# Performance work log

Hardware: AMD Instinct MI355X
Metric: run time of the kernel (lower is better)

The kernel has to match this reference:

```python
import jax, jax.numpy as jnp
import numpy as np

NUM_HEADS = 16
NEG_INF = -1e30


def setup_inputs() -> dict:
    key = jax.random.key(0)
    k1, k2, k3 = jax.random.split(key, 3)
    B, S, D = 2, 2048, 1024
    x = jax.random.normal(k1, (B, S, D), dtype=jnp.float32)
    # torch Linear(D, 3D, bias=False) stored here already transposed: y = x @ w_qkv
    w_qkv = jax.random.normal(k2, (D, 3 * D), dtype=jnp.float32) * 0.02
    w_out = jax.random.normal(k3, (D, D), dtype=jnp.float32) * 0.02
    return {"x": x, "w_qkv": w_qkv, "w_out": w_out}


def reference(x, w_qkv, w_out):
    B, S, D = x.shape
    H = NUM_HEADS
    dh = D // H
    qkv = x @ w_qkv                      # [B, S, 3D]
    q, k, v = jnp.split(qkv, 3, axis=-1)

    def to_heads(t):
        return t.reshape(B, S, H, dh).transpose(0, 2, 1, 3)  # [B, H, S, dh]

    q, k, v = to_heads(q), to_heads(k), to_heads(v)
    scale = jnp.asarray(dh, x.dtype) ** -0.5
    scores = jnp.einsum('bhqd,bhkd->bhqk', q, k) * scale     # [B, H, S, S]
    causal = jnp.tril(jnp.ones((S, S), dtype=bool))
    scores = jnp.where(causal, scores, NEG_INF)
    attn = jax.nn.softmax(scores, axis=-1)
    out = jnp.einsum('bhqk,bhkd->bhqd', attn, v)             # [B, H, S, dh]
    out = out.transpose(0, 2, 1, 3).reshape(B, S, D)
    return out @ w_out
```

## Files before the change

### kernel.cpp

```cpp
#include <hip/hip_runtime.h>

typedef unsigned short u16;
typedef unsigned int u32;

typedef __bf16 bf16x8 __attribute__((ext_vector_type(8)));
typedef _Float16 f16x8 __attribute__((ext_vector_type(8)));
typedef float f32x4 __attribute__((ext_vector_type(4)));
typedef float f32x16 __attribute__((ext_vector_type(16)));
typedef u32 u32x4 __attribute__((ext_vector_type(4)));

typedef __attribute__((address_space(1))) u32 as1_u32;
typedef __attribute__((address_space(3))) u32 as3_u32;

#define EKF 0.18033688011112042f

__device__ __forceinline__ u16 f2bf(float x) {
  u32 u = __float_as_uint(x);
  u = u + 0x7fffu + ((u >> 16) & 1u);
  return (u16)(u >> 16);
}
__device__ __forceinline__ u32 pack2(float a, float b) {
  return (u32)f2bf(a) | ((u32)f2bf(b) << 16);
}
__device__ __forceinline__ u32 pkf16(float a, float b) {
  return __builtin_bit_cast(u32, __builtin_amdgcn_cvt_pkrtz(a, b));
}
__device__ __forceinline__ u16 f2h(float a) {
  return (u16)(pkf16(a, a) & 0xffffu);
}
__device__ __forceinline__ void gld_lds16(const u16* g, const u16* l) {
  __builtin_amdgcn_global_load_lds((const as1_u32*)g, (as3_u32*)l, 16, 0, 0);
}

__global__ __launch_bounds__(256) void prepass_kernel(const float* __restrict__ x,
                                                      const float* __restrict__ w_qkv,
                                                      const float* __restrict__ w_out,
                                                      u16* __restrict__ xb,
                                                      u16* __restrict__ wqkvT,
                                                      u16* __restrict__ woutT) {
  __shared__ float tile[64][65];
  int bid = blockIdx.x;
  int t = threadIdx.x;
  if (bid < 4096) {
    int i = bid * 256 + t;
    float4 v = ((const float4*)x)[i];
    uint2 r;
    r.x = pack2(v.x, v.y);
    r.y = pack2(v.z, v.w);
    ((uint2*)xb)[i] = r;
    return;
  }
  const float* W;
  u16* WT;
  int K, N, bx, by;
  if (bid < 4096 + 768) {
    int b2 = bid - 4096;
    W = w_qkv; WT = wqkvT; K = 1024; N = 3072; bx = b2 & 15; by = b2 >> 4;
  } else {
    int b2 = bid - 4864;
    W = w_out; WT = woutT; K = 1024; N = 1024; bx = b2 & 15; by = b2 >> 4;
  }
  int k0 = bx * 64, n0 = by * 64;
  int r = t >> 4, c4 = (t & 15) * 4;
#pragma unroll
  for (int i = 0; i < 4; ++i) {
    int row = r + i * 16;
    float4 v = *(const float4*)&W[(size_t)(k0 + row) * N + n0 + c4];
    tile[row][c4 + 0] = v.x; tile[row][c4 + 1] = v.y;
    tile[row][c4 + 2] = v.z; tile[row][c4 + 3] = v.w;
  }
  __syncthreads();
#pragma unroll
  for (int i = 0; i < 4; ++i) {
    int n = r + i * 16;
    uint2 o;
    o.x = pack2(tile[c4 + 0][n], tile[c4 + 1][n]);
    o.y = pack2(tile[c4 + 2][n], tile[c4 + 3][n]);
    *(uint2*)&WT[(size_t)(n0 + n) * K + k0 + c4] = o;
  }
}

__global__ __launch_bounds__(512, 2) void gemm_qkv256_kernel(const u16* __restrict__ A,
                                                             const u16* __restrict__ BT,
                                                             u16* __restrict__ QK,
                                                             u16* __restrict__ VT) {
  __shared__ __attribute__((aligned(16))) u16 smem[57344];
  const int tid = threadIdx.x;
  const int wave = tid >> 6;
  const int lane = tid & 63;
  const int lr = lane & 15;
  const int kg = lane >> 4;
  const int l7 = lr & 7;
  const int wr = wave >> 2;
  const int wc = wave & 3;

  int b = blockIdx.x;
  int sw = (b & 7) * 32 + (b >> 3);
  const int bm = (sw >> 4) * 256;
  const int bn = (sw & 15) * 192;

  const int srow = tid >> 3;
  const int scg = ((tid & 7) ^ (srow & 7)) * 8;
  const u16* pa = A + (size_t)(bm + srow) * 1024 + scg;
  const u16* pb = BT + (size_t)(bn + srow) * 1024 + scg;
  const u32 lw = (u32)wave * 512;

  f32x4 acc[8][3];
#pragma unroll
  for (int i = 0; i < 8; ++i)
#pragma unroll
    for (int j = 0; j < 3; ++j) {
      f32x4 z = {0.f, 0.f, 0.f, 0.f};
      acc[i][j] = z;
    }

  {
    u16* dA = (u16*)smem;
    u16* dB = (u16*)smem + 16384;
#pragma unroll
    for (int i = 0; i < 4; ++i) gld_lds16(pa + (size_t)(i * 64) * 1024, dA + lw + i * 4096);
#pragma unroll
    for (int i = 0; i < 3; ++i) gld_lds16(pb + (size_t)(i * 64) * 1024, dB + lw + i * 4096);
  }

  for (int t = 0; t < 16; ++t) {
    __syncthreads();
    const u16* bA = smem + (t & 1) * 28672;
    const u16* bB = bA + 16384;
    if (t + 1 < 16) {
      u16* dA = (u16*)smem + ((t + 1) & 1) * 28672;
      u16* dB = dA + 16384;
      const int k1 = (t + 1) * 64;
#pragma unroll
      for (int i = 0; i < 4; ++i) gld_lds16(pa + (size_t)(i * 64) * 1024 + k1, dA + lw + i * 4096);
#pragma unroll
      for (int i = 0; i < 3; ++i) gld_lds16(pb + (size_t)(i * 64) * 1024 + k1, dB + lw + i * 4096);
    }
    bf16x8 bfr[2][3];
#pragma unroll
    for (int kh = 0; kh < 2; ++kh)
#pragma unroll
      for (int ni = 0; ni < 3; ++ni)
        bfr[kh][ni] = *(const bf16x8*)(bB + (wc * 48 + ni * 16 + lr) * 64 +
                                       (((kh * 4 + kg) ^ l7) * 8));
#pragma unroll
    for (int ph = 0; ph < 4; ++ph) {
      const int mh = ph >> 1, kh = ph & 1;
      bf16x8 af[4];
#pragma unroll
      for (int mi = 0; mi < 4; ++mi)
        af[mi] = *(const bf16x8*)(bA + (wr * 128 + mh * 64 + mi * 16 + lr) * 64 +
                                  (((kh * 4 + kg) ^ l7) * 8));
      __builtin_amdgcn_s_barrier();
      __builtin_amdgcn_s_setprio(1);
#pragma unroll
      for (int mi = 0; mi < 4; ++mi)
#pragma unroll
        for (int ni = 0; ni < 3; ++ni)
          acc[mh * 4 + mi][ni] = __builtin_amdgcn_mfma_f32_16x16x32_bf16(
              bfr[kh][ni], af[mi], acc[mh * 4 + mi][ni], 0, 0, 0);
      __builtin_amdgcn_s_setprio(0);
      __builtin_amdgcn_s_barrier();
    }
  }

  __syncthreads();
#pragma unroll
  for (int i = 0; i < 8; ++i)
#pragma unroll
    for (int ni = 0; ni < 3; ++ni) {
      const int coff = wc * 48 + ni * 16 + kg * 4;
      const int cglob = bn + coff;
      f32x4 a = acc[i][ni];
      if (cglob >= 2048) {
        int r = bm + wr * 128 + i * 16 + lr;
        int cc = cglob - 2048;
        int bh2 = (r >> 11) * 16 + (cc >> 6);
        int j = r & 2047;
        u16* vrow = VT + ((size_t)bh2 * 64 + (cc & 63)) * 2048 + j;
#pragma unroll
        for (int rr = 0; rr < 4; ++rr) vrow[(size_t)rr * 2048] = f2h(a[rr]);
      } else {
        float scale = (cglob < 1024) ? EKF : 1.0f;
        int row = wr * 128 + i * 16 + lr;
        int chunk = coff >> 2;
        u32 off = (u32)row * 192 + (u32)((chunk ^ (row & 6)) << 2);
        *(uint2*)((u16*)smem + off) =
            make_uint2(pack2(a[0] * scale, a[1] * scale), pack2(a[2] * scale, a[3] * scale));
      }
    }
  __syncthreads();
  if (bn < 2048) {
#pragma unroll
    for (int i2 = 0; i2 < 16; ++i2) {
      int row = i2 * 16 + (tid >> 5);
      int lc = tid & 31;
      if (lc < 24 && bn + lc * 8 < 2048) {
        uint4 v = *(const uint4*)((const u16*)smem + (u32)row * 192 +
                                  (u32)(((2 * lc) ^ (row & 6)) * 4));
        *(uint4*)(QK + (size_t)(bm + row) * 2048 + bn + lc * 8) = v;
      }
    }
  }
}

__global__ __launch_bounds__(256, 2) void gemm_out_kernel(const u16* __restrict__ A,
                                                          const u16* __restrict__ BT,
                                                          float* __restrict__ C) {
  __shared__ __attribute__((aligned(16))) u16 smem[2][12288];
  const int tid = threadIdx.x;
  const int wave = tid >> 6;
  const int lane = tid & 63;
  const int lr = lane & 15;
  const int kg = lane >> 4;
  const int lr7 = lr & 7;
  const int wm = (wave >> 1) * 32;
  const int wn = (wave & 1) * 64;

  const int b = blockIdx.x;
  const int xcd = b & 7, loc = b >> 3;
  const int bm = (xcd * 8 + (loc >> 3)) * 64;
  const int bn = (loc & 7) * 128;

  const int sr = tid >> 3;
  const int scg = ((tid & 7) ^ (sr & 7)) * 8;
  const u16* pa = A + (size_t)(bm + sr) * 1024 + scg;
  const u16* pb = BT + (size_t)(bn + sr) * 1024 + scg;
  const u32 lw = (u32)wave * 512;

  f32x4 acc[2][4];
#pragma unroll
  for (int i = 0; i < 2; ++i)
#pragma unroll
    for (int j = 0; j < 4; ++j) {
      f32x4 z = {0.f, 0.f, 0.f, 0.f};
      acc[i][j] = z;
    }

  {
    u16* dA = smem[0];
    u16* dB = smem[0] + 4096;
#pragma unroll
    for (int i = 0; i < 2; ++i) gld_lds16(pa + (size_t)(i * 32) * 1024, dA + lw + i * 2048);
#pragma unroll
    for (int i = 0; i < 4; ++i) gld_lds16(pb + (size_t)(i * 32) * 1024, dB + lw + i * 2048);
  }

  for (int t = 0; t < 16; ++t) {
    __syncthreads();
    const u16* bA = smem[t & 1];
    const u16* bB = bA + 4096;
    if (t + 1 < 16) {
      u16* dA = smem[(t + 1) & 1];
      u16* dB = dA + 4096;
      const int k1 = (t + 1) * 64;
#pragma unroll
      for (int i = 0; i < 2; ++i) gld_lds16(pa + (size_t)(i * 32) * 1024 + k1, dA + lw + i * 2048);
#pragma unroll
      for (int i = 0; i < 4; ++i) gld_lds16(pb + (size_t)(i * 32) * 1024 + k1, dB + lw + i * 2048);
    }
#pragma unroll
    for (int kk = 0; kk < 2; ++kk) {
      const int ch = ((kk * 4 + kg) ^ lr7) * 8;
      bf16x8 af[2], bfr[4];
#pragma unroll
      for (int mi = 0; mi < 2; ++mi)
        af[mi] = *(const bf16x8*)(bA + (wm + mi * 16 + lr) * 64 + ch);
#pragma unroll
      for (int ni = 0; ni < 4; ++ni)
        bfr[ni] = *(const bf16x8*)(bB + (wn + ni * 16 + lr) * 64 + ch);
      __builtin_amdgcn_s_setprio(1);
#pragma unroll
      for (int mi = 0; mi < 2; ++mi)
#pragma unroll
        for (int ni = 0; ni < 4; ++ni)
          acc[mi][ni] = __builtin_amdgcn_mfma_f32_16x16x32_bf16(bfr[ni], af[mi], acc[mi][ni], 0, 0, 0);
      __builtin_amdgcn_s_setprio(0);
    }
  }

  float* buf = (float*)smem;
#pragma unroll
  for (int hc = 0; hc < 2; ++hc) {
    __syncthreads();
    if ((wave & 1) == hc) {
#pragma unroll
      for (int mi = 0; mi < 2; ++mi)
#pragma unroll
        for (int ni = 0; ni < 4; ++ni) {
          int row = wm + mi * 16 + lr;
          int cp = ((ni * 4 + kg) ^ lr) * 4;
          *(f32x4*)(buf + row * 64 + cp) = acc[mi][ni];
        }
    }
    __syncthreads();
#pragma unroll
    for (int i = 0; i < 4; ++i) {
      int row = i * 16 + (tid >> 4);
      int lc = tid & 15;
      float4 v = *(const float4*)(buf + row * 64 + ((lc ^ (row & 15)) * 4));
      *(float4*)(C + (size_t)(bm + row) * 1024 + bn + hc * 64 + lc * 4) = v;
    }
  }
}

__global__ __launch_bounds__(256, 4) void attn_mfma_kernel(const u16* __restrict__ qk,
                                                           const u16* __restrict__ vt,
                                                           u16* __restrict__ out) {
  __shared__ __attribute__((aligned(16))) u16 sK[2][64 * 64];
  __shared__ __attribute__((aligned(16))) u16 sV[2][64 * 64];

  const int tid = threadIdx.x;
  const int wave = tid >> 6;
  const int lane = tid & 63;
  const int l31 = lane & 31;
  const int hi = lane >> 5;
  const int qh = wave & 1;
  const int jh = wave >> 1;

  int idx = blockIdx.x;
  int qi = 31 - (idx >> 5);
  int bh = (idx & 7) * 4 + ((idx >> 3) & 3);
  int b = bh >> 4, h = bh & 15;
  int q0 = qi * 64;

  const u16* qbase = qk + (size_t)b * 2048 * 2048 + h * 64;
  const u16* kbase = qbase + 1024;
  const u16* vbase = vt + (size_t)bh * 64 * 2048;
  u16* obase = out + (size_t)b * 2048 * 1024 + h * 64;

  const int sra = wave * 16 + (lane >> 3);
  const int srb = sra + 8;
  const int sc = lane & 7;
  const u32 koffA = (u32)sra * 2048 + (u32)((sc ^ (sra & 7)) * 8);
  const u32 koffB = (u32)srb * 2048 + (u32)((sc ^ (srb & 7)) * 8);
  const u32 ldsA = (wave * 2 + 0) * 512;
  const u32 ldsB = (wave * 2 + 1) * 512;

  const int qcol = q0 + qh * 32 + l31;
  bf16x8 qf[4];
  {
    const u16* qrow = qbase + (size_t)qcol * 2048;
#pragma unroll
    for (int s = 0; s < 4; ++s) qf[s] = *(const bf16x8*)(qrow + s * 16 + hi * 8);
  }

  f32x16 oacc[2];
#pragma unroll
  for (int i = 0; i < 16; ++i) { oacc[0][i] = 0.f; oacc[1][i] = 0.f; }
  float ls = 0.f;

  const int nrounds = qi + 1;
  gld_lds16(kbase + koffA, sK[0] + ldsA);
  gld_lds16(kbase + koffB, sK[0] + ldsB);
  gld_lds16(vbase + koffA, sV[0] + ldsA);
  gld_lds16(vbase + koffB, sV[0] + ldsB);
  __syncthreads();

  for (int t = 0; t < nrounds; ++t) {
    if (t + 1 < nrounds) {
      int j1 = (t + 1) * 64;
      u16* dK = sK[(t + 1) & 1];
      u16* dV = sV[(t + 1) & 1];
      gld_lds16(kbase + (size_t)j1 * 2048 + koffA, dK + ldsA);
      gld_lds16(kbase + (size_t)j1 * 2048 + koffB, dK + ldsB);
      gld_lds16(vbase + j1 + koffA, dV + ldsA);
      gld_lds16(vbase + j1 + koffB, dV + ldsB);
    }
    const u16* sKb = sK[t & 1];
    const u16* sVb = sV[t & 1];
    const bool diag = (t == qi);

    f32x16 c;
#pragma unroll
    for (int i = 0; i < 16; ++i) c[i] = 0.f;
#pragma unroll
    for (int s = 0; s < 4; ++s) {
      const u32 row = (u32)(jh * 32 + l31);
      bf16x8 kf = *(const bf16x8*)(sKb + row * 64 + (((2 * s + hi) ^ (row & 7)) * 8));
      c = __builtin_amdgcn_mfma_f32_32x32x16_bf16(kf, qf[s], c, 0, 0, 0);
    }
    float p[16];
    const int qrel = qh * 32 + l31;
#pragma unroll
    for (int r = 0; r < 16; ++r) {
      int joff = jh * 32 + (r & 3) + 8 * (r >> 2) + 4 * hi;
      float e = exp2f(c[r]);
      p[r] = (!diag || (joff <= qrel)) ? e : 0.f;
    }
    {
      float s0 = (p[0] + p[1]) + (p[2] + p[3]);
      float s1 = (p[4] + p[5]) + (p[6] + p[7]);
      float s2 = (p[8] + p[9]) + (p[10] + p[11]);
      float s3 = (p[12] + p[13]) + (p[14] + p[15]);
      ls += (s0 + s1) + (s2 + s3);
    }
    u32 c01 = pkf16(p[0], p[1]),   c23 = pkf16(p[2], p[3]);
    u32 c45 = pkf16(p[4], p[5]),   c67 = pkf16(p[6], p[7]);
    u32 c89 = pkf16(p[8], p[9]),   cab = pkf16(p[10], p[11]);
    u32 ccd = pkf16(p[12], p[13]), cef = pkf16(p[14], p[15]);
    asm volatile("v_permlane32_swap_b32 %0, %1" : "+v"(c01), "+v"(c45));
    asm volatile("v_permlane32_swap_b32 %0, %1" : "+v"(c23), "+v"(c67));
    asm volatile("v_permlane32_swap_b32 %0, %1" : "+v"(c89), "+v"(ccd));
    asm volatile("v_permlane32_swap_b32 %0, %1" : "+v"(cab), "+v"(cef));
    u32x4 w0 = {c01, c23, c45, c67};
    u32x4 w1 = {c89, cab, ccd, cef};
    f16x8 pa0 = __builtin_bit_cast(f16x8, w0);
    f16x8 pa1 = __builtin_bit_cast(f16x8, w1);

    __builtin_amdgcn_s_setprio(1);
#pragma unroll
    for (int dh = 0; dh < 2; ++dh) {
      const u32 row = (u32)(dh * 32 + l31);
#pragma unroll
      for (int s2 = 0; s2 < 2; ++s2) {
        f16x8 vf = *(const f16x8*)(sVb + row * 64 +
                                   (((4 * jh + 2 * s2 + hi) ^ (row & 7)) * 8));
        oacc[dh] = __builtin_amdgcn_mfma_f32_32x32x16_f16(
            vf, (s2 == 0) ? pa0 : pa1, oacc[dh], 0, 0, 0);
      }
    }
    __builtin_amdgcn_s_setprio(0);
    __syncthreads();
  }

  ls += __shfl_xor(ls, 32);

  float* obuf = (float*)sK;
  float* lbuf = (float*)sV;
  const int q = qh * 32 + l31;
  if (jh == 1) {
#pragma unroll
    for (int dh = 0; dh < 2; ++dh)
#pragma unroll
      for (int g = 0; g < 4; ++g) {
        int ch = dh * 8 + g * 2 + hi;
        f32x4 w = {oacc[dh][4 * g + 0], oacc[dh][4 * g + 1],
                   oacc[dh][4 * g + 2], oacc[dh][4 * g + 3]};
        *(f32x4*)(obuf + q * 64 + ((ch ^ (q & 15)) * 4)) = w;
      }
    if (hi == 0) lbuf[q] = ls;
  }
  __syncthreads();
  if (jh == 0) {
    float inv = 1.0f / (ls + lbuf[q]);
    u16* orow = obase + (size_t)qcol * 1024;
#pragma unroll
    for (int dh = 0; dh < 2; ++dh)
#pragma unroll
      for (int g = 0; g < 4; ++g) {
        int ch = dh * 8 + g * 2 + hi;
        f32x4 po = *(const f32x4*)(obuf + q * 64 + ((ch ^ (q & 15)) * 4));
        float o0 = (oacc[dh][4 * g + 0] + po[0]) * inv;
        float o1 = (oacc[dh][4 * g + 1] + po[1]) * inv;
        float o2 = (oacc[dh][4 * g + 2] + po[2]) * inv;
        float o3 = (oacc[dh][4 * g + 3] + po[3]) * inv;
        *(uint2*)(orow + dh * 32 + g * 8 + hi * 4) = make_uint2(pack2(o0, o1), pack2(o2, o3));
      }
  }
}

extern "C" void kernel_launch(void* const* d_in, const int* in_sizes, int n_in,
                              void* d_out, int out_size, void* d_ws, size_t ws_size,
                              hipStream_t stream) {
  const float* x = (const float*)d_in[0];
  const float* w_qkv = (const float*)d_in[1];
  const float* w_out = (const float*)d_in[2];
  float* out = (float*)d_out;

  char* ws = (char*)d_ws;
  u16* xb    = (u16*)(ws);
  u16* wqkvT = (u16*)(ws + (8u << 20));
  u16* woutT = (u16*)(ws + (14u << 20));
  u16* qkb   = (u16*)(ws + (16u << 20));
  u16* vtb   = (u16*)(ws + (32u << 20));
  u16* attn  = (u16*)(ws + (40u << 20));

  prepass_kernel<<<5120, 256, 0, stream>>>(x, w_qkv, w_out, xb, wqkvT, woutT);

  gemm_qkv256_kernel<<<256, 512, 0, stream>>>(xb, wqkvT, qkb, vtb);

  attn_mfma_kernel<<<1024, 256, 0, stream>>>(qkb, vtb, attn);

  gemm_out_kernel<<<512, 256, 0, stream>>>(attn, woutT, out);
}
```

Before: 160.5 us.

## Shrink QKV GEMM tile to 128 rows and drop intra-tile barriers

The QKV projection GEMM tile drops from 256x192 to 128x192, so 512 blocks are launched instead of 256 and shared memory per block is smaller, allowing higher occupancy (launch bounds raised to 4). The inner loop is simplified to two k-halves without the per-phase s_barrier synchronisation, and the block-to-tile mapping is changed to group rows per XCD. This aims to fill the 256 CUs better and cut barrier stalls, at the cost of less B-tile reuse per loaded A and more global traffic for the weight tile.

```diff
diff --git a/kernel.cpp b/kernel.cpp
--- a/kernel.cpp
+++ b/kernel.cpp
@@ -80,11 +80,11 @@
   }
 }
 
-__global__ __launch_bounds__(512, 2) void gemm_qkv256_kernel(const u16* __restrict__ A,
+__global__ __launch_bounds__(512, 4) void gemm_qkv128_kernel(const u16* __restrict__ A,
                                                              const u16* __restrict__ BT,
                                                              u16* __restrict__ QK,
                                                              u16* __restrict__ VT) {
-  __shared__ __attribute__((aligned(16))) u16 smem[57344];
+  __shared__ __attribute__((aligned(16))) u16 smem[40960];
   const int tid = threadIdx.x;
   const int wave = tid >> 6;
   const int lane = tid & 63;
@@ -94,10 +94,10 @@
   const int wr = wave >> 2;
   const int wc = wave & 3;
 
-  int b = blockIdx.x;
-  int sw = (b & 7) * 32 + (b >> 3);
-  const int bm = (sw >> 4) * 256;
-  const int bn = (sw & 15) * 192;
+  const int b = blockIdx.x;
+  const int xcd = b & 7, loc = b >> 3;
+  const int bm = (xcd * 4 + (loc >> 4)) * 128;
+  const int bn = (loc & 15) * 192;
 
   const int srow = tid >> 3;
   const int scg = ((tid & 7) ^ (srow & 7)) * 8;
@@ -105,9 +105,9 @@
   const u16* pb = BT + (size_t)(bn + srow) * 1024 + scg;
   const u32 lw = (u32)wave * 512;
 
-  f32x4 acc[8][3];
-#pragma unroll
-  for (int i = 0; i < 8; ++i)
+  f32x4 acc[4][3];
+#pragma unroll
+  for (int i = 0; i < 4; ++i)
 #pragma unroll
     for (int j = 0; j < 3; ++j) {
       f32x4 z = {0.f, 0.f, 0.f, 0.f};
@@ -116,64 +116,56 @@
 
   {
     u16* dA = (u16*)smem;
-    u16* dB = (u16*)smem + 16384;
-#pragma unroll
-    for (int i = 0; i < 4; ++i) gld_lds16(pa + (size_t)(i * 64) * 1024, dA + lw + i * 4096);
+    u16* dB = (u16*)smem + 8192;
+#pragma unroll
+    for (int i = 0; i < 2; ++i) gld_lds16(pa + (size_t)(i * 64) * 1024, dA + lw + i * 4096);
 #pragma unroll
     for (int i = 0; i < 3; ++i) gld_lds16(pb + (size_t)(i * 64) * 1024, dB + lw + i * 4096);
   }
 
   for (int t = 0; t < 16; ++t) {
     __syncthreads();
-    const u16* bA = smem + (t & 1) * 28672;
-    const u16* bB = bA + 16384;
+    const u16* bA = smem + (t & 1) * 20480;
+    const u16* bB = bA + 8192;
     if (t + 1 < 16) {
-      u16* dA = (u16*)smem + ((t + 1) & 1) * 28672;
-      u16* dB = dA + 16384;
+      u16* dA = (u16*)smem + ((t + 1) & 1) * 20480;
+      u16* dB = dA + 8192;
       const int k1 = (t + 1) * 64;
 #pragma unroll
-      for (int i = 0; i < 4; ++i) gld_lds16(pa + (size_t)(i * 64) * 1024 + k1, dA + lw + i * 4096);
+      for (int i = 0; i < 2; ++i) gld_lds16(pa + (size_t)(i * 64) * 1024 + k1, dA + lw + i * 4096);
 #pragma unroll
       for (int i = 0; i < 3; ++i) gld_lds16(pb + (size_t)(i * 64) * 1024 + k1, dB + lw + i * 4096);
     }
-    bf16x8 bfr[2][3];
-#pragma unroll
-    for (int kh = 0; kh < 2; ++kh)
+#pragma unroll
+    for (int kk = 0; kk < 2; ++kk) {
+      const int ch = ((kk * 4 + kg) ^ l7) * 8;
+      bf16x8 af[4], bfr[3];
+#pragma unroll
+      for (int mi = 0; mi < 4; ++mi)
+        af[mi] = *(const bf16x8*)(bA + (wr * 64 + mi * 16 + lr) * 64 + ch);
 #pragma unroll
       for (int ni = 0; ni < 3; ++ni)
-        bfr[kh][ni] = *(const bf16x8*)(bB + (wc * 48 + ni * 16 + lr) * 64 +
-                                       (((kh * 4 + kg) ^ l7) * 8));
-#pragma unroll
-    for (int ph = 0; ph < 4; ++ph) {
-      const int mh = ph >> 1, kh = ph & 1;
-      bf16x8 af[4];
+        bfr[ni] = *(const bf16x8*)(bB + (wc * 48 + ni * 16 + lr) * 64 + ch);
+      __builtin_amdgcn_s_setprio(1);
 #pragma unroll
       for (int mi = 0; mi < 4; ++mi)
-        af[mi] = *(const bf16x8*)(bA + (wr * 128 + mh * 64 + mi * 16 + lr) * 64 +
-                                  (((kh * 4 + kg) ^ l7) * 8));
-      __builtin_amdgcn_s_barrier();
-      __builtin_amdgcn_s_setprio(1);
-#pragma unroll
-      for (int mi = 0; mi < 4; ++mi)
 #pragma unroll
         for (int ni = 0; ni < 3; ++ni)
-          acc[mh * 4 + mi][ni] = __builtin_amdgcn_mfma_f32_16x16x32_bf16(
-              bfr[kh][ni], af[mi], acc[mh * 4 + mi][ni], 0, 0, 0);
+          acc[mi][ni] = __builtin_amdgcn_mfma_f32_16x16x32_bf16(bfr[ni], af[mi], acc[mi][ni], 0, 0, 0);
       __builtin_amdgcn_s_setprio(0);
-      __builtin_amdgcn_s_barrier();
     }
   }
 
   __syncthreads();
 #pragma unroll
-  for (int i = 0; i < 8; ++i)
+  for (int i = 0; i < 4; ++i)
 #pragma unroll
     for (int ni = 0; ni < 3; ++ni) {
       const int coff = wc * 48 + ni * 16 + kg * 4;
       const int cglob = bn + coff;
       f32x4 a = acc[i][ni];
       if (cglob >= 2048) {
-        int r = bm + wr * 128 + i * 16 + lr;
+        int r = bm + wr * 64 + i * 16 + lr;
         int cc = cglob - 2048;
         int bh2 = (r >> 11) * 16 + (cc >> 6);
         int j = r & 2047;
@@ -182,7 +174,7 @@
         for (int rr = 0; rr < 4; ++rr) vrow[(size_t)rr * 2048] = f2h(a[rr]);
       } else {
         float scale = (cglob < 1024) ? EKF : 1.0f;
-        int row = wr * 128 + i * 16 + lr;
+        int row = wr * 64 + i * 16 + lr;
         int chunk = coff >> 2;
         u32 off = (u32)row * 192 + (u32)((chunk ^ (row & 6)) << 2);
         *(uint2*)((u16*)smem + off) =
@@ -192,7 +184,7 @@
   __syncthreads();
   if (bn < 2048) {
 #pragma unroll
-    for (int i2 = 0; i2 < 16; ++i2) {
+    for (int i2 = 0; i2 < 8; ++i2) {
       int row = i2 * 16 + (tid >> 5);
       int lc = tid & 31;
       if (lc < 24 && bn + lc * 8 < 2048) {
@@ -478,7 +470,7 @@
 
   prepass_kernel<<<5120, 256, 0, stream>>>(x, w_qkv, w_out, xb, wqkvT, woutT);
 
-  gemm_qkv256_kernel<<<256, 512, 0, stream>>>(xb, wqkvT, qkb, vtb);
+  gemm_qkv128_kernel<<<512, 512, 0, stream>>>(xb, wqkvT, qkb, vtb);
 
   attn_mfma_kernel<<<1024, 256, 0, stream>>>(qkb, vtb, attn);
 
```

New measurement: 157.6 us. Within noise of the previous version (-1.8%).
